# Performance work log

Hardware: AMD Instinct MI355X
Metric: run time of the kernel (lower is better)

Reference implementation:

```python
import jax, jax.numpy as jnp
import numpy as np

N, E, B = 100000, 3200000, 64   # nodes, edges, graphs
F_IN, F_OUT, N_OUT = 20, 20, 5


def setup_inputs() -> dict:
    key = jax.random.key(0)
    ks = jax.random.split(key, 9)
    x = jax.random.normal(ks[0], (N, F_IN), jnp.float32)
    edge_index = jax.random.randint(ks[1], (2, E), 0, N, dtype=jnp.int32)
    batch = jnp.sort(jax.random.randint(ks[2], (N,), 0, B, dtype=jnp.int32))
    s = 1.0 / np.sqrt(F_IN)
    W = jax.random.normal(ks[3], (F_IN, F_OUT), jnp.float32) * s       # GAT linear
    att_src = jax.random.normal(ks[4], (F_OUT,), jnp.float32) * s      # a_src (heads=1)
    att_dst = jax.random.normal(ks[5], (F_OUT,), jnp.float32) * s      # a_dst
    bias = jax.random.normal(ks[6], (F_OUT,), jnp.float32) * 0.01
    out_W = jax.random.normal(ks[7], (F_OUT, N_OUT), jnp.float32) * s
    out_b = jax.random.normal(ks[8], (N_OUT,), jnp.float32) * 0.01
    return {"x": x, "edge_index": edge_index, "batch": batch, "W": W,
            "att_src": att_src, "att_dst": att_dst, "bias": bias,
            "out_W": out_W, "out_b": out_b}


def reference(x, edge_index, batch, W, att_src, att_dst, bias, out_W, out_b):
    n = x.shape[0]
    # PyG GATConv default: add self-loops
    loop = jnp.arange(n, dtype=edge_index.dtype)
    src = jnp.concatenate([edge_index[0], loop])
    dst = jnp.concatenate([edge_index[1], loop])

    h = x @ W                                   # [N, F_OUT]
    a_s = h @ att_src                           # [N]
    a_d = h @ att_dst                           # [N]
    # per-edge attention logit, LeakyReLU(0.2) as in PyG GATConv
    e = jax.nn.leaky_relu(a_s[src] + a_d[dst], negative_slope=0.2)
    # segment softmax over incoming edges of each destination node
    m = jax.ops.segment_max(e, dst, num_segments=n)
    ex = jnp.exp(e - m[dst])
    den = jax.ops.segment_sum(ex, dst, num_segments=n)
    alpha = ex / den[dst]                       # [E+N]  (dropout inactive in eval)
    agg = jax.ops.segment_sum(alpha[:, None] * h[src], dst, num_segments=n) + bias

    xact = jax.nn.leaky_relu(agg, negative_slope=0.01)   # nn.LeakyReLU default
    # global mean pool per graph
    cnt = jax.ops.segment_sum(jnp.ones((n,), xact.dtype), batch, num_segments=B)
    pooled = jax.ops.segment_sum(xact, batch, num_segments=B) / jnp.maximum(cnt, 1.0)[:, None]
    logits = pooled @ out_W + out_b             # [B, 5]
    return jax.nn.softmax(logits, axis=-1)
```

## Files before the change

### kernel.cpp

```cpp
#include <hip/hip_runtime.h>
#include <math.h>

#define F_IN 20
#define F_OUT 20
#define N_OUT 5
#define NPB 64
#define NPB_SH 6
#define HSW 8
#define CAPMAX 2816
#define NBINMAX 1600
#define CHUNK 13056
#define SPMAX 4

typedef float floatx2 __attribute__((ext_vector_type(2)));
#define PK8(a, b, old, hi) __builtin_amdgcn_cvt_pk_fp8_f32((a), (b), (int)(old), (hi))
#define UPK8(u, hi)        __builtin_amdgcn_cvt_pk_f32_fp8((int)(u), (hi))

__global__ __launch_bounds__(1024) void k1a_fused(
    const float* __restrict__ x, const float* __restrict__ W,
    const float* __restrict__ att_s, const float* __restrict__ att_d,
    unsigned* __restrict__ hpack, float* __restrict__ a_d,
    const int* __restrict__ ei, int* __restrict__ gcur,
    unsigned int* __restrict__ bdata,
    int n, int E, int nbuck, int cap, int k1blocks)
{
    __shared__ union {
        struct { float sW[F_IN * F_OUT]; float sas[F_OUT]; float sad[F_OUT]; } lin;
        struct { int hist[NBINMAX]; int incl[NBINMAX]; int curb[NBINMAX];
                 unsigned sbuf[CHUNK]; } bin;
    } u;

    int tid = threadIdx.x;

    if (blockIdx.x < k1blocks) {
        for (int i = tid; i < F_IN * F_OUT; i += 1024) u.lin.sW[i] = W[i];
        if (tid < F_OUT) { u.lin.sas[tid] = att_s[tid]; u.lin.sad[tid] = att_d[tid]; }
        __syncthreads();

        int i = blockIdx.x * 1024 + tid;
        if (i >= n) return;

        float xi[F_IN];
        const float4* xp = (const float4*)(x + (size_t)i * F_IN);
#pragma unroll
        for (int q = 0; q < F_IN / 4; ++q) {
            float4 v = xp[q];
            xi[4 * q + 0] = v.x; xi[4 * q + 1] = v.y;
            xi[4 * q + 2] = v.z; xi[4 * q + 3] = v.w;
        }

        float hrow[F_OUT];
        float as_acc = 0.f, ad_acc = 0.f;
#pragma unroll
        for (int j = 0; j < F_OUT; ++j) {
            float hj = 0.f;
#pragma unroll
            for (int k = 0; k < F_IN; ++k) hj += xi[k] * u.lin.sW[k * F_OUT + j];
            hrow[j] = hj;
            as_acc += hj * u.lin.sas[j];
            ad_acc += hj * u.lin.sad[j];
        }

        unsigned rw[5];
#pragma unroll
        for (int j = 0; j < 5; ++j) {
            unsigned t = PK8(hrow[4 * j + 0], hrow[4 * j + 1], 0u, false);
            rw[j]      = PK8(hrow[4 * j + 2], hrow[4 * j + 3], t,  true);
        }

        uint4* hp = (uint4*)(hpack + (size_t)i * HSW);
        uint4 v0; v0.x = rw[0]; v0.y = rw[1]; v0.z = rw[2]; v0.w = rw[3];
        uint4 v1; v1.x = rw[4]; v1.y = __float_as_uint(as_acc); v1.z = 0u; v1.w = 0u;
        hp[0] = v0;
        hp[1] = v1;
        a_d[i] = ad_acc;
    } else {
        int bb    = blockIdx.x - k1blocks;
        int start = bb * CHUNK;
        int chunk = min(CHUNK, E - start);
        if (chunk <= 0) return;
        const int* dsts = ei + E;

        for (int b = tid; b < nbuck; b += 1024) { u.bin.hist[b] = 0; u.bin.curb[b] = 0; }
        __syncthreads();

        for (int e = tid; e < chunk; e += 1024)
            atomicAdd(&u.bin.hist[dsts[start + e] >> NPB_SH], 1);
        __syncthreads();

        int b0 = 2 * tid, b1 = 2 * tid + 1;
        int h0 = (b0 < nbuck) ? u.bin.hist[b0] : 0;
        int h1 = (b1 < nbuck) ? u.bin.hist[b1] : 0;
        int psum = h0 + h1;
        u.bin.incl[tid] = psum;
        __syncthreads();
        for (int s = 1; s < 1024; s <<= 1) {
            int v = (tid >= s) ? u.bin.incl[tid - s] : 0;
            __syncthreads();
            u.bin.incl[tid] += v;
            __syncthreads();
        }
        int excl = u.bin.incl[tid] - psum;
        __syncthreads();
        if (b0 < nbuck) u.bin.incl[b0] = excl + h0;
        if (b1 < nbuck) u.bin.incl[b1] = excl + h0 + h1;
        __syncthreads();

        for (int e = tid; e < chunk; e += 1024) {
            int d = dsts[start + e];
            int s = ei[start + e];
            int b = d >> NPB_SH;
            int pos = u.bin.incl[b] - u.bin.hist[b] + atomicAdd(&u.bin.curb[b], 1);
            u.bin.sbuf[pos] = ((unsigned)s << NPB_SH) | (unsigned)(d & (NPB - 1));
        }
        __syncthreads();

        for (int b = tid; b < nbuck; b += 1024) {
            int c = u.bin.hist[b];
            u.bin.curb[b] = c ? atomicAdd(&gcur[b], c) : 0;
        }
        __syncthreads();

        for (int p = tid; p < chunk; p += 1024) {
            unsigned w = u.bin.sbuf[p];
            int lo = 0, hi = nbuck;
            while (lo < hi) {
                int m = (lo + hi) >> 1;
                if (u.bin.incl[m] <= p) lo = m + 1; else hi = m;
            }
            int b  = lo;
            int st = u.bin.incl[b] - u.bin.hist[b];
            int gpos = u.bin.curb[b] + (p - st);
            if (gpos < cap) bdata[(size_t)b * cap + gpos] = w;
        }
    }
}

__global__ __launch_bounds__(256) void kb_srt(const int* __restrict__ gcur,
                                              const unsigned int* __restrict__ bdata,
                                              const unsigned* __restrict__ hpack,
                                              const float* __restrict__ a_d,
                                              const float* __restrict__ bias,
                                              const int* __restrict__ batch,
                                              float* __restrict__ pooled,
                                              int n, int cap)
{
    __shared__ int   sent[CAPMAX];
    __shared__ int   hist[NPB];
    __shared__ int   incl[NPB];
    __shared__ int   cur[NPB];
    __shared__ float adl[NPB];
    __shared__ int   sbatch[NPB];
    __shared__ float sbias[F_OUT];
    __shared__ float spool[SPMAX * F_OUT];

    int b = blockIdx.x;
    int node_lo = b << NPB_SH;
    int nn = min(NPB, n - node_lo);
    int tid = threadIdx.x;

    if (tid < NPB) { hist[tid] = 0; cur[tid] = 0; }
    if (tid < nn) {
        adl[tid] = a_d[node_lo + tid];
        sbatch[tid] = batch[node_lo + tid];
    }
    if (tid < F_OUT) sbias[tid] = bias[tid];
    if (tid < SPMAX * F_OUT) spool[tid] = 0.f;
    __syncthreads();

    int cnt = min(gcur[b], cap);
    const unsigned int* bd = bdata + (size_t)b * cap;

    for (int e = tid; e < cnt; e += 256)
        atomicAdd(&hist[bd[e] & (NPB - 1)], 1);
    __syncthreads();

    if (tid < NPB) incl[tid] = hist[tid];
    __syncthreads();
#pragma unroll
    for (int s = 1; s < NPB; s <<= 1) {
        int v = 0;
        if (tid < NPB && tid >= s) v = incl[tid - s];
        __syncthreads();
        if (tid < NPB) incl[tid] += v;
        __syncthreads();
    }

    for (int e = tid; e < cnt; e += 256) {
        unsigned w = bd[e];
        int ldst = (int)(w & (NPB - 1));
        int pos = incl[ldst] - hist[ldst] + atomicAdd(&cur[ldst], 1);
        sent[pos] = (int)(w >> NPB_SH);
    }
    __syncthreads();

    int node = tid >> 2, sub = tid & 3;
    float acc[21];
#pragma unroll
    for (int f = 0; f < 21; ++f) acc[f] = 0.f;

    if (node < nn) {
        int start = incl[node] - hist[node];
        int end   = incl[node];
        float ad  = adl[node];
        for (int k = start + sub; k < end; k += 4) {
            int src = sent[k];
            const uint4* rp = (const uint4*)(hpack + (size_t)src * HSW);
            uint4 r0 = rp[0], r1 = rp[1];
            float as = __uint_as_float(r1.y);
            float vv = as + ad;
            vv = vv > 0.f ? vv : 0.2f * vv;
            float ex = __expf(vv);
            floatx2 f;
            f = UPK8(r0.x, false); acc[0]  += ex * f.x; acc[1]  += ex * f.y;
            f = UPK8(r0.x, true);  acc[2]  += ex * f.x; acc[3]  += ex * f.y;
            f = UPK8(r0.y, false); acc[4]  += ex * f.x; acc[5]  += ex * f.y;
            f = UPK8(r0.y, true);  acc[6]  += ex * f.x; acc[7]  += ex * f.y;
            f = UPK8(r0.z, false); acc[8]  += ex * f.x; acc[9]  += ex * f.y;
            f = UPK8(r0.z, true);  acc[10] += ex * f.x; acc[11] += ex * f.y;
            f = UPK8(r0.w, false); acc[12] += ex * f.x; acc[13] += ex * f.y;
            f = UPK8(r0.w, true);  acc[14] += ex * f.x; acc[15] += ex * f.y;
            f = UPK8(r1.x, false); acc[16] += ex * f.x; acc[17] += ex * f.y;
            f = UPK8(r1.x, true);  acc[18] += ex * f.x; acc[19] += ex * f.y;
            acc[20] += ex;
        }
    }

#pragma unroll
    for (int f = 0; f < 21; ++f) {
        acc[f] += __shfl_xor(acc[f], 1);
        acc[f] += __shfl_xor(acc[f], 2);
    }

    if (node < nn && sub == 0) {
        int i = node_lo + node;
        const uint4* rp = (const uint4*)(hpack + (size_t)i * HSW);
        uint4 r0 = rp[0], r1 = rp[1];
        float vv = __uint_as_float(r1.y) + adl[node];
        vv = vv > 0.f ? vv : 0.2f * vv;
        float exs = __expf(vv);
        float inv = 1.f / (acc[20] + exs);

        float hs[F_OUT];
        floatx2 f;
        f = UPK8(r0.x, false); hs[0]  = f.x; hs[1]  = f.y;
        f = UPK8(r0.x, true);  hs[2]  = f.x; hs[3]  = f.y;
        f = UPK8(r0.y, false); hs[4]  = f.x; hs[5]  = f.y;
        f = UPK8(r0.y, true);  hs[6]  = f.x; hs[7]  = f.y;
        f = UPK8(r0.z, false); hs[8]  = f.x; hs[9]  = f.y;
        f = UPK8(r0.z, true);  hs[10] = f.x; hs[11] = f.y;
        f = UPK8(r0.w, false); hs[12] = f.x; hs[13] = f.y;
        f = UPK8(r0.w, true);  hs[14] = f.x; hs[15] = f.y;
        f = UPK8(r1.x, false); hs[16] = f.x; hs[17] = f.y;
        f = UPK8(r1.x, true);  hs[18] = f.x; hs[19] = f.y;

        float v[F_OUT];
#pragma unroll
        for (int ff = 0; ff < F_OUT; ++ff) {
            float t = (acc[ff] + exs * hs[ff]) * inv + sbias[ff];
            v[ff] = t > 0.f ? t : 0.01f * t;
        }

        int gl = sbatch[node] - sbatch[0];
        if (gl < SPMAX) {
#pragma unroll
            for (int ff = 0; ff < F_OUT; ++ff) atomicAdd(&spool[gl * F_OUT + ff], v[ff]);
        } else {
#pragma unroll
            for (int ff = 0; ff < F_OUT; ++ff)
                atomicAdd(&pooled[(size_t)sbatch[node] * F_OUT + ff], v[ff]);
        }
    }
    __syncthreads();

    int g0 = sbatch[0];
    int ngl = min(SPMAX, sbatch[nn - 1] - g0 + 1);
    for (int idx = tid; idx < ngl * F_OUT; idx += 256)
        atomicAdd(&pooled[(size_t)(g0 + idx / F_OUT) * F_OUT + idx % F_OUT], spool[idx]);
}

__global__ void k4_head(const float* __restrict__ pooled, const int* __restrict__ batch,
                        const float* __restrict__ out_W, const float* __restrict__ out_b,
                        float* __restrict__ out, int B, int n)
{
    int g = blockIdx.x * blockDim.x + threadIdx.x;
    if (g >= B) return;

    int bnd[2];
#pragma unroll
    for (int t = 0; t < 2; ++t) {
        int target = g + t;
        int lo = 0, hi = n;
        while (lo < hi) {
            int m = (lo + hi) >> 1;
            if (batch[m] < target) lo = m + 1; else hi = m;
        }
        bnd[t] = lo;
    }
    float cntf = (float)(bnd[1] - bnd[0]);
    float invc = 1.f / (cntf > 1.f ? cntf : 1.f);

    float p[F_OUT];
#pragma unroll
    for (int f = 0; f < F_OUT; ++f) p[f] = pooled[(size_t)g * F_OUT + f] * invc;

    float lg[N_OUT];
#pragma unroll
    for (int o = 0; o < N_OUT; ++o) {
        float acc = out_b[o];
#pragma unroll
        for (int f = 0; f < F_OUT; ++f) acc += p[f] * out_W[f * N_OUT + o];
        lg[o] = acc;
    }
    float m = lg[0];
#pragma unroll
    for (int o = 1; o < N_OUT; ++o) m = lg[o] > m ? lg[o] : m;
    float s = 0.f;
#pragma unroll
    for (int o = 0; o < N_OUT; ++o) { lg[o] = expf(lg[o] - m); s += lg[o]; }
    float inv = 1.f / s;
#pragma unroll
    for (int o = 0; o < N_OUT; ++o) out[g * N_OUT + o] = lg[o] * inv;
}

extern "C" void kernel_launch(void* const* d_in, const int* in_sizes, int n_in,
                              void* d_out, int out_size, void* d_ws, size_t ws_size,
                              hipStream_t stream)
{
    const float* x       = (const float*)d_in[0];
    const int*   ei      = (const int*)  d_in[1];
    const int*   batch   = (const int*)  d_in[2];
    const float* W       = (const float*)d_in[3];
    const float* att_src = (const float*)d_in[4];
    const float* att_dst = (const float*)d_in[5];
    const float* bias    = (const float*)d_in[6];
    const float* out_W   = (const float*)d_in[7];
    const float* out_b   = (const float*)d_in[8];
    float* out = (float*)d_out;

    int n = in_sizes[0] / F_IN;
    int E = in_sizes[1] / 2;
    int B = out_size / N_OUT;

    int nbuck = (n + NPB - 1) >> NPB_SH;
    int avg   = E / nbuck;
    int cap   = avg + avg / 4 + 256;
    if (cap > CAPMAX) cap = CAPMAX;

    char* ws = (char*)d_ws;
    unsigned* hpack = (unsigned*)ws;   ws += (size_t)n * HSW * 4;
    float* a_d      = (float*)ws;      ws += (size_t)n * 4;
    int*   gcur     = (int*)ws;        ws += (size_t)nbuck * 4;
    float* pooled   = (float*)ws;      ws += (size_t)B * F_OUT * 4;
    ws = (char*)(((size_t)ws + 15) & ~(size_t)15);
    unsigned int* bdata = (unsigned int*)ws;  ws += (size_t)nbuck * cap * 4;

    hipMemsetAsync(gcur, 0, (size_t)nbuck * 4 + (size_t)B * F_OUT * 4, stream);

    int k1blocks = (n + 1023) / 1024;
    int nbb      = (E + CHUNK - 1) / CHUNK;

    k1a_fused<<<k1blocks + nbb, 1024, 0, stream>>>(
        x, W, att_src, att_dst, hpack, a_d, ei, gcur, bdata,
        n, E, nbuck, cap, k1blocks);
    kb_srt   <<<nbuck, 256, 0, stream>>>(gcur, bdata, hpack, a_d, bias, batch,
                                         pooled, n, cap);
    k4_head  <<<1, 64, 0, stream>>>(pooled, batch, out_W, out_b, out, B, n);
}
```

Measured before the change: 166.8 us.

## Split each destination bucket across two blocks with eight threads per node

The gather/aggregate kernel now launches two blocks per 64-node bucket. Each block handles 32 destination nodes and filters the bucket's packed edges down to its own half. Within a block, eight lanes now share each node instead of four, and a third shuffle stage is added to the reduction. The aim is more parallelism and more in-flight gathers per node. The cost is that each bucket's edge list is read twice for histogramming and scattering. The bucket capacity is also rounded up to a multiple of four.

Measured after the change: 173.4 us. 4.0% more time.

```diff
diff --git a/kernel.cpp b/kernel.cpp
--- a/kernel.cpp
+++ b/kernel.cpp
@@ -6,6 +6,7 @@
 #define N_OUT 5
 #define NPB 64
 #define NPB_SH 6
+#define NPH 32
 #define HSW 8
 #define CAPMAX 2816
 #define NBINMAX 1600
@@ -146,20 +147,22 @@
                                               int n, int cap)
 {
     __shared__ int   sent[CAPMAX];
-    __shared__ int   hist[NPB];
-    __shared__ int   incl[NPB];
-    __shared__ int   cur[NPB];
-    __shared__ float adl[NPB];
-    __shared__ int   sbatch[NPB];
+    __shared__ int   hist[NPH];
+    __shared__ int   incl[NPH];
+    __shared__ int   cur[NPH];
+    __shared__ float adl[NPH];
+    __shared__ int   sbatch[NPH];
     __shared__ float sbias[F_OUT];
     __shared__ float spool[SPMAX * F_OUT];
 
-    int b = blockIdx.x;
-    int node_lo = b << NPB_SH;
-    int nn = min(NPB, n - node_lo);
+    int bucket = blockIdx.x >> 1;
+    int half   = blockIdx.x & 1;
+    int node_lo = (bucket << NPB_SH) + (half << 5);
+    int nn = min(NPH, n - node_lo);
+    if (nn <= 0) return;
     int tid = threadIdx.x;
 
-    if (tid < NPB) { hist[tid] = 0; cur[tid] = 0; }
+    if (tid < NPH) { hist[tid] = 0; cur[tid] = 0; }
     if (tid < nn) {
         adl[tid] = a_d[node_lo + tid];
         sbatch[tid] = batch[node_lo + tid];
@@ -168,33 +171,38 @@
     if (tid < SPMAX * F_OUT) spool[tid] = 0.f;
     __syncthreads();
 
-    int cnt = min(gcur[b], cap);
-    const unsigned int* bd = bdata + (size_t)b * cap;
-
-    for (int e = tid; e < cnt; e += 256)
-        atomicAdd(&hist[bd[e] & (NPB - 1)], 1);
-    __syncthreads();
-
-    if (tid < NPB) incl[tid] = hist[tid];
-    __syncthreads();
-#pragma unroll
-    for (int s = 1; s < NPB; s <<= 1) {
+    int cnt = min(gcur[bucket], cap);
+    const unsigned int* bd = bdata + (size_t)bucket * cap;
+
+    for (int e = tid; e < cnt; e += 256) {
+        int ldst = (int)(bd[e] & (NPB - 1));
+        if ((ldst >> 5) == half) atomicAdd(&hist[ldst & (NPH - 1)], 1);
+    }
+    __syncthreads();
+
+    if (tid < NPH) incl[tid] = hist[tid];
+    __syncthreads();
+#pragma unroll
+    for (int s = 1; s < NPH; s <<= 1) {
         int v = 0;
-        if (tid < NPB && tid >= s) v = incl[tid - s];
-        __syncthreads();
-        if (tid < NPB) incl[tid] += v;
+        if (tid < NPH && tid >= s) v = incl[tid - s];
+        __syncthreads();
+        if (tid < NPH) incl[tid] += v;
         __syncthreads();
     }
 
     for (int e = tid; e < cnt; e += 256) {
         unsigned w = bd[e];
         int ldst = (int)(w & (NPB - 1));
-        int pos = incl[ldst] - hist[ldst] + atomicAdd(&cur[ldst], 1);
-        sent[pos] = (int)(w >> NPB_SH);
-    }
-    __syncthreads();
-
-    int node = tid >> 2, sub = tid & 3;
+        if ((ldst >> 5) == half) {
+            int lb = ldst & (NPH - 1);
+            int pos = incl[lb] - hist[lb] + atomicAdd(&cur[lb], 1);
+            sent[pos] = (int)(w >> NPB_SH);
+        }
+    }
+    __syncthreads();
+
+    int node = tid >> 3, sub = tid & 7;
     float acc[21];
 #pragma unroll
     for (int f = 0; f < 21; ++f) acc[f] = 0.f;
@@ -203,7 +211,7 @@
         int start = incl[node] - hist[node];
         int end   = incl[node];
         float ad  = adl[node];
-        for (int k = start + sub; k < end; k += 4) {
+        for (int k = start + sub; k < end; k += 8) {
             int src = sent[k];
             const uint4* rp = (const uint4*)(hpack + (size_t)src * HSW);
             uint4 r0 = rp[0], r1 = rp[1];
@@ -230,6 +238,7 @@
     for (int f = 0; f < 21; ++f) {
         acc[f] += __shfl_xor(acc[f], 1);
         acc[f] += __shfl_xor(acc[f], 2);
+        acc[f] += __shfl_xor(acc[f], 4);
     }
 
     if (node < nn && sub == 0) {
@@ -345,6 +354,7 @@
     int nbuck = (n + NPB - 1) >> NPB_SH;
     int avg   = E / nbuck;
     int cap   = avg + avg / 4 + 256;
+    cap = (cap + 3) & ~3;
     if (cap > CAPMAX) cap = CAPMAX;
 
     char* ws = (char*)d_ws;
@@ -363,7 +373,7 @@
     k1a_fused<<<k1blocks + nbb, 1024, 0, stream>>>(
         x, W, att_src, att_dst, hpack, a_d, ei, gcur, bdata,
         n, E, nbuck, cap, k1blocks);
-    kb_srt   <<<nbuck, 256, 0, stream>>>(gcur, bdata, hpack, a_d, bias, batch,
-                                         pooled, n, cap);
+    kb_srt   <<<nbuck * 2, 256, 0, stream>>>(gcur, bdata, hpack, a_d, bias, batch,
+                                             pooled, n, cap);
     k4_head  <<<1, 64, 0, stream>>>(pooled, batch, out_W, out_b, out, B, n);
 }
```
